# Kernel tuning notes

Hardware: AMD Instinct MI355X
Metric: run time of the kernel (lower is better)

## Reference

```python
import math
import jax, jax.numpy as jnp
import numpy as np

B, L, D = 2, 2048, 512
H, DK, RANK, NH = 8, 64, 32, 1
K_MAX = 64
BANDWIDTH = 8.0
N_BUCKETS = 16


def setup_inputs() -> dict:
    key = jax.random.key(0)
    ks = jax.random.split(key, 14)
    s = 0.02
    return {
        "query": jax.random.normal(ks[0], (B, L, D), jnp.float32),
        "key": jax.random.normal(ks[1], (B, L, D), jnp.float32),
        "value": jax.random.normal(ks[2], (B, L, D), jnp.float32),
        "Wq": jax.random.normal(ks[3], (D, H * DK), jnp.float32) * s,
        "bq": jnp.zeros((H * DK,), jnp.float32),
        "Wk": jax.random.normal(ks[4], (D, H * DK), jnp.float32) * s,
        "bk": jnp.zeros((H * DK,), jnp.float32),
        "Wv": jax.random.normal(ks[5], (D, H * DK), jnp.float32) * s,
        "bv": jnp.zeros((H * DK,), jnp.float32),
        "U": jax.random.normal(ks[6], (H, DK, RANK), jnp.float32) * s,
        "V": jax.random.normal(ks[7], (H, RANK, D), jnp.float32) * s,
        "rv": jax.random.normal(ks[8], (H, DK, NH), jnp.float32),  # LSH random vectors (buffer)
        "Wo": jax.random.normal(ks[9], (H * D, D), jnp.float32) * s,
        "bo": jnp.zeros((D,), jnp.float32),
    }


def _lsh_hash(x, r):
    # binary quantize then bucketed floor hash: [B,L,dk] @ [dk,nh] -> [B,L,nh]
    xb = (x > 0).astype(x.dtype)
    return jnp.floor((xb @ r) / BANDWIDTH) % N_BUCKETS


def reference(query, key, value, Wq, bq, Wk, bk, Wv, bv, U, V, rv, Wo, bo):
    Bq, Lq, Dm = query.shape
    nheads, dk = U.shape[0], U.shape[1]
    q = (query @ Wq + bq).reshape(Bq, Lq, nheads, dk).transpose(0, 2, 1, 3)  # [B,H,L,dk]
    k = (key @ Wk + bk).reshape(Bq, Lq, nheads, dk).transpose(0, 2, 1, 3)
    v = (value @ Wv + bv).reshape(Bq, Lq, nheads, dk).transpose(0, 2, 1, 3)
    scale = math.sqrt(dk)  # optimized_sqrt(d_key), d_key power of two

    head_outputs = []
    for h in range(nheads):
        qh, kh, vh = q[:, h], k[:, h], v[:, h]  # [B,L,dk]
        qhash = _lsh_hash(qh, rv[h])  # [B,L,nh]
        khash = _lsh_hash(kh, rv[h])
        # [B,L,L] candidate match matrix (all hashes equal)
        matches = (qhash[:, :, None, :] == khash[:, None, :, :]).all(-1)
        # first K_MAX matching key indices in ascending order (== torch nonzero order)
        order = jnp.argsort(jnp.logical_not(matches), axis=-1, stable=True)
        cand = order[:, :, :K_MAX]  # [B,L,k_max]
        valid = jnp.take_along_axis(matches, cand, axis=-1)  # [B,L,k_max]
        ckeys = jnp.take_along_axis(kh[:, None, :, :], cand[..., None], axis=2)  # [B,L,k_max,dk]
        cvals = jnp.take_along_axis(vh[:, None, :, :], cand[..., None], axis=2)
        sim = jnp.einsum('bld,blkd->blk', qh, ckeys) / scale
        sim = jnp.where(valid, sim, -jnp.inf)
        attn = jax.nn.softmax(sim, axis=-1)  # invalid slots get exactly 0 weight
        # attention-weighted sum then low-rank up-projection (linear, so commutes
        # with the weighted sum; avoids the [B,L,k_max,d_model] intermediate)
        ctx = jnp.einsum('blk,blkd->bld', attn, cvals)  # [B,L,dk]
        head_outputs.append((ctx @ U[h]) @ V[h])  # [B,L,d_model]

    concat = jnp.concatenate(head_outputs, axis=-1)  # [B,L,H*d_model]
    return concat @ Wo + bo
```

## Files before the change

### kernel.cpp

```cpp
#include <hip/hip_runtime.h>
#include <math.h>

#define Bb 2
#define Ll 2048
#define Dd 512
#define Hh 8
#define DKq 64
#define NBUCK 16
#define KMAX 64
#define MAX_ITEMS 1280

__device__ __forceinline__ void gl_lds16(const float* g, float* l) {
  __builtin_amdgcn_global_load_lds(
      (const __attribute__((address_space(1))) void*)g,
      (__attribute__((address_space(3))) void*)l, 16, 0, 0);
}

__global__ __launch_bounds__(128) void proj_kernel(
    const float* __restrict__ Xq, const float* __restrict__ Xk, const float* __restrict__ Xv,
    const float* __restrict__ Wq, const float* __restrict__ Wk, const float* __restrict__ Wv,
    const float* __restrict__ bq, const float* __restrict__ bk, const float* __restrict__ bv,
    float* __restrict__ qb, float* __restrict__ kb, float* __restrict__ vb)
{
  const float *X, *W, *bias; float* dst;
  if (blockIdx.z == 0)      { X=Xq; W=Wq; bias=bq; dst=qb; }
  else if (blockIdx.z == 1) { X=Xk; W=Wk; bias=bk; dst=kb; }
  else                      { X=Xv; W=Wv; bias=bv; dst=vb; }
  __shared__ float As[2][64 * 32];
  __shared__ float Bs[2][32 * 128];
  const int tid = threadIdx.x;
  const int m0 = blockIdx.y * 64;
  const int n0 = blockIdx.x * 128;
  const int tx = tid & 15, ty = tid >> 4;
  const int lane = tid & 63, wid = tid >> 6;

  const float* aSrc[4];
  #pragma unroll
  for (int j = 0; j < 4; j++) {
    int jj = wid * 4 + j;
    aSrc[j] = X + (size_t)(m0 + 8*jj + (lane >> 3)) * 512 + (((lane & 7) ^ jj) << 2);
  }
  const float* bSrc[8];
  #pragma unroll
  for (int j = 0; j < 8; j++) {
    int jj = wid * 8 + j;
    bSrc[j] = W + (size_t)(2*jj + (lane >> 5)) * 512 + n0 + ((lane & 31) << 2);
  }

  #pragma unroll
  for (int j = 0; j < 4; j++) gl_lds16(aSrc[j],            &As[0][(wid*4+j)*256]);
  #pragma unroll
  for (int j = 0; j < 8; j++) gl_lds16(bSrc[j],            &Bs[0][(wid*8+j)*256]);
  __syncthreads();

  float acc[8][8] = {};
  for (int t = 0; t < 16; t++) {
    const int cur = t & 1;
    if (t < 15) {
      const int k0 = (t + 1) * 32;
      #pragma unroll
      for (int j = 0; j < 4; j++) gl_lds16(aSrc[j] + k0,              &As[cur^1][(wid*4+j)*256]);
      #pragma unroll
      for (int j = 0; j < 8; j++) gl_lds16(bSrc[j] + (size_t)k0*512,  &Bs[cur^1][(wid*8+j)*256]);
    }
    const float* Ac = &As[cur][0];
    const float* Bc = &Bs[cur][0];
    #pragma unroll
    for (int kk4 = 0; kk4 < 8; kk4++) {
      float4 a[8];
      #pragma unroll
      for (int i = 0; i < 8; i++)
        a[i] = *(const float4*)&Ac[(ty*8 + i)*32 + ((kk4 ^ ty) << 2)];
      #pragma unroll
      for (int s = 0; s < 4; s++) {
        const int kk = kk4*4 + s;
        float4 b0 = *(const float4*)&Bc[kk*128 + tx*4];
        float4 b1 = *(const float4*)&Bc[kk*128 + 64 + tx*4];
        #pragma unroll
        for (int i = 0; i < 8; i++) {
          const float as = (s==0) ? a[i].x : (s==1) ? a[i].y : (s==2) ? a[i].z : a[i].w;
          acc[i][0] += as * b0.x;  acc[i][1] += as * b0.y;
          acc[i][2] += as * b0.z;  acc[i][3] += as * b0.w;
          acc[i][4] += as * b1.x;  acc[i][5] += as * b1.y;
          acc[i][6] += as * b1.z;  acc[i][7] += as * b1.w;
        }
      }
    }
    __syncthreads();
  }

  const int head0 = n0 >> 6;
  const int d0 = tx * 4;
  #pragma unroll
  for (int i = 0; i < 8; i++) {
    int m = m0 + ty*8 + i;
    int b = m >> 11, l = m & 2047;
    float* drow0 = &dst[(((size_t)b*Hh + head0)*Ll + l)*DKq];
    float* drow1 = &dst[(((size_t)b*Hh + head0 + 1)*Ll + l)*DKq];
    #pragma unroll
    for (int j = 0; j < 4; j++) drow0[d0 + j] = acc[i][j]   + bias[n0 + tx*4 + j];
    #pragma unroll
    for (int j = 0; j < 4; j++) drow1[d0 + j] = acc[i][4+j] + bias[n0 + 64 + tx*4 + j];
  }
}

__global__ __launch_bounds__(256) void hash_kernel(
    const float* __restrict__ qb, const float* __restrict__ kb,
    const float* __restrict__ rv, int* __restrict__ qhash, int* __restrict__ khash)
{
  int gwave = (blockIdx.x * blockDim.x + threadIdx.x) >> 6;
  int lane = threadIdx.x & 63;
  const int NR = Bb * Hh * Ll;
  if (gwave >= 2 * NR) return;
  int isK = gwave >= NR;
  int row = isK ? gwave - NR : gwave;
  int h = (row >> 11) & 7;
  const float* src = isK ? kb : qb;
  float x = src[(size_t)row * DKq + lane];
  float r = rv[h * DKq + lane];
  float v = (x > 0.0f) ? r : 0.0f;
  #pragma unroll
  for (int off = 32; off; off >>= 1) v += __shfl_xor(v, off);
  if (lane == 0) {
    float fb = floorf(v * 0.125f);
    int ib = (int)fb;
    int bucket = ib & 15;
    (isK ? khash : qhash)[row] = bucket;
  }
}

__global__ __launch_bounds__(64) void kcand_kernel(
    const int* __restrict__ khash, int* __restrict__ kcand, int* __restrict__ kcount)
{
  int bh = blockIdx.x >> 4;
  int bucket = blockIdx.x & 15;
  int lane = threadIdx.x;
  const int* kh = &khash[bh * Ll];
  int* cl = &kcand[(size_t)blockIdx.x * KMAX];
  int total = 0;
  for (int c0 = 0; c0 < Ll && total < KMAX; c0 += 64) {
    int hv = kh[c0 + lane];
    unsigned long long m = __ballot(hv == bucket);
    int pre = __popcll(m & ((1ULL << lane) - 1ULL));
    if (hv == bucket && total + pre < KMAX) cl[total + pre] = c0 + lane;
    total += __popcll(m);
  }
  if (lane == 0) kcount[blockIdx.x] = total < KMAX ? total : KMAX;
}

__global__ __launch_bounds__(256) void qlist_kernel(
    const int* __restrict__ qhash, int* __restrict__ qoff, int* __restrict__ qlist)
{
  int bh = blockIdx.x;
  __shared__ int cnt[NBUCK], cur[NBUCK], off[NBUCK + 1];
  if (threadIdx.x < NBUCK) cnt[threadIdx.x] = 0;
  __syncthreads();
  const int* qh = &qhash[bh * Ll];
  for (int l = threadIdx.x; l < Ll; l += 256) atomicAdd(&cnt[qh[l]], 1);
  __syncthreads();
  if (threadIdx.x == 0) {
    int s = 0;
    for (int i = 0; i < NBUCK; i++) { off[i] = s; cur[i] = s; s += cnt[i]; }
    off[NBUCK] = s;
  }
  __syncthreads();
  if (threadIdx.x < NBUCK + 1) qoff[bh * (NBUCK + 1) + threadIdx.x] = off[threadIdx.x];
  for (int l = threadIdx.x; l < Ll; l += 256) {
    int p = atomicAdd(&cur[qh[l]], 1);
    qlist[bh * Ll + p] = l;
  }
}

__global__ __launch_bounds__(256) void worklist_kernel(
    const int* __restrict__ qoff, const int* __restrict__ kcount,
    int4* __restrict__ items, int* __restrict__ nitems)
{
  int t = threadIdx.x;
  int bh = t >> 4, bucket = t & 15;
  int o0 = qoff[bh * 17 + bucket], o1 = qoff[bh * 17 + bucket + 1];
  int cnt = kcount[t];
  int nq = o1 - o0;
  int n = (cnt > 0) ? ((nq + 31) >> 5) : 0;
  __shared__ int sc[256];
  sc[t] = n;
  __syncthreads();
  for (int off = 1; off < 256; off <<= 1) {
    int v = (t >= off) ? sc[t - off] : 0;
    __syncthreads();
    sc[t] += v;
    __syncthreads();
  }
  int start = sc[t] - n;
  for (int i = 0; i < n; i++) {
    int q0 = 32 * i;
    int qn = nq - q0; if (qn > 32) qn = 32;
    items[start + i] = make_int4(t, o0 + q0, qn, cnt);
  }
  if (t == 255) nitems[0] = sc[255];
}

__device__ __forceinline__ void lds_fence() {
  asm volatile("s_waitcnt lgkmcnt(0)" ::: "memory");
  __builtin_amdgcn_sched_barrier(0);
}

__global__ __launch_bounds__(256, 2) void attn_kernel(
    const float* __restrict__ qb, const float* __restrict__ kb, const float* __restrict__ vb,
    const int* __restrict__ qlist, const int* __restrict__ kcand,
    const int4* __restrict__ items, const int* __restrict__ nitems,
    float* __restrict__ ctx)
{
  __shared__ float qs_all[4][32 * 64];
  __shared__ float sa_all[4][64];
  const int wid = threadIdx.x >> 6, lane = threadIdx.x & 63;
  const int idx = blockIdx.x * 4 + wid;
  if (idx >= nitems[0]) return;
  const int4 it = items[idx];
  const int code = it.x, qstart = it.y, qn = it.z, cnt = it.w;
  const int bh = code >> 4;
  float* qs = qs_all[wid];
  float* sa = sa_all[wid];

  const float* qbh = qb + (size_t)bh * Ll * DKq;
  const float* kbh = kb + (size_t)bh * Ll * DKq;
  const float* vbh = vb + (size_t)bh * Ll * DKq;

  int qidx_v = (lane < qn)  ? qlist[bh * Ll + qstart + lane] : 0;
  int cidx_v = (lane < cnt) ? kcand[(size_t)code * KMAX + lane] : 0;

  float4 kr[16];
  {
    const float4* krow = (const float4*)kbh + (size_t)cidx_v * 16;
    #pragma unroll
    for (int i = 0; i < 16; i++) kr[i] = krow[i];
  }
  float vt[64];
  #pragma unroll
  for (int c = 0; c < 64; c++) {
    int rowc = __shfl(cidx_v, c);
    vt[c] = vbh[(size_t)rowc * DKq + lane];
  }
  #pragma unroll
  for (int i = 0; i < 8; i++) {
    int f = lane + 64 * i;
    int r = f >> 4, c4 = f & 15;
    int qrow = __shfl(qidx_v, r);
    float4 qv = *((const float4*)qbh + (size_t)qrow * 16 + c4);
    *(float4*)&qs[r * 64 + c4 * 4] = qv;
  }
  lds_fence();

  const int b = bh >> 3, h = bh & 7;
  const float4* qs4 = (const float4*)qs;
  const float4* sa4 = (const float4*)sa;

  for (int j = 0; j < qn; j++) {
    float s0 = 0.f, s1 = 0.f, s2 = 0.f, s3 = 0.f;
    #pragma unroll
    for (int i = 0; i < 16; i += 4) {
      float4 q0 = qs4[j * 16 + i + 0];
      float4 q1 = qs4[j * 16 + i + 1];
      float4 q2 = qs4[j * 16 + i + 2];
      float4 q3 = qs4[j * 16 + i + 3];
      s0 += q0.x*kr[i+0].x + q0.y*kr[i+0].y + q0.z*kr[i+0].z + q0.w*kr[i+0].w;
      s1 += q1.x*kr[i+1].x + q1.y*kr[i+1].y + q1.z*kr[i+1].z + q1.w*kr[i+1].w;
      s2 += q2.x*kr[i+2].x + q2.y*kr[i+2].y + q2.z*kr[i+2].z + q2.w*kr[i+2].w;
      s3 += q3.x*kr[i+3].x + q3.y*kr[i+3].y + q3.z*kr[i+3].z + q3.w*kr[i+3].w;
    }
    float s = ((s0 + s1) + (s2 + s3)) * 0.125f;
    s = (lane < cnt) ? s : -INFINITY;
    float m = s;
    #pragma unroll
    for (int off = 32; off; off >>= 1) m = fmaxf(m, __shfl_xor(m, off));
    float e = __expf(s - m);
    float sum = e;
    #pragma unroll
    for (int off = 32; off; off >>= 1) sum += __shfl_xor(sum, off);
    lds_fence();
    sa[lane] = e;
    lds_fence();
    float c0 = 0.f, c1 = 0.f, c2 = 0.f, c3 = 0.f;
    #pragma unroll
    for (int i = 0; i < 16; i++) {
      float4 a = sa4[i];
      c0 += a.x * vt[4*i + 0];
      c1 += a.y * vt[4*i + 1];
      c2 += a.z * vt[4*i + 2];
      c3 += a.w * vt[4*i + 3];
    }
    float ctxd = ((c0 + c1) + (c2 + c3)) / sum;
    int qrow = __shfl(qidx_v, j);
    ctx[((size_t)(b * Ll + qrow)) * 512 + h * 64 + lane] = ctxd;
  }
}

__global__ __launch_bounds__(256) void uv_kernel(
    const float* __restrict__ U, const float* __restrict__ V, float* __restrict__ T)
{
  int idx = blockIdx.x * 256 + threadIdx.x;
  int n = idx & 511, dk = (idx >> 9) & 63, h = idx >> 15;
  float acc = 0.f;
  #pragma unroll
  for (int r = 0; r < 32; r++)
    acc += U[((size_t)h * 64 + dk) * 32 + r] * V[((size_t)h * 32 + r) * 512 + n];
  T[idx] = acc;
}

__global__ __launch_bounds__(256) void m_kernel(
    const float* __restrict__ T, const float* __restrict__ Wo, float* __restrict__ Mf)
{
  __shared__ float Ts[16][68];
  __shared__ float Ws[16][68];
  const int h = blockIdx.y;
  const int n0 = blockIdx.x * 64;
  const int tid = threadIdx.x;
  const int tx = tid & 15, ty = tid >> 4;
  float acc[4][4] = {};
  for (int k0 = 0; k0 < 512; k0 += 16) {
    {
      int r = tid >> 2, cg = (tid & 3) << 2;
      float4 a = *(const float4*)&T[((size_t)(h*64 + r))*512 + k0 + cg];
      Ts[cg+0][r]=a.x; Ts[cg+1][r]=a.y; Ts[cg+2][r]=a.z; Ts[cg+3][r]=a.w;
    }
    {
      int row = tid >> 4, c4 = tid & 15;
      *(float4*)&Ws[row][c4*4] = *(const float4*)&Wo[((size_t)(h*512 + k0 + row))*512 + n0 + c4*4];
    }
    __syncthreads();
    #pragma unroll
    for (int kk = 0; kk < 16; kk++) {
      float4 a0 = *(const float4*)&Ts[kk][ty*4];
      float4 b0 = *(const float4*)&Ws[kk][tx*4];
      float av[4] = {a0.x,a0.y,a0.z,a0.w};
      float bw[4] = {b0.x,b0.y,b0.z,b0.w};
      #pragma unroll
      for (int i=0;i<4;i++)
        #pragma unroll
        for (int j=0;j<4;j++) acc[i][j] += av[i]*bw[j];
    }
    __syncthreads();
  }
  #pragma unroll
  for (int i=0;i<4;i++) {
    int row = h*64 + ty*4 + i;
    #pragma unroll
    for (int j=0;j<4;j++)
      Mf[(size_t)row * 512 + n0 + tx*4 + j] = acc[i][j];
  }
}

__global__ __launch_bounds__(128) void out_gemm(
    const float* __restrict__ A, const float* __restrict__ Bm,
    const float* __restrict__ bias, float* __restrict__ C)
{
  __shared__ float As[32][68];
  __shared__ float Bs[32][68];
  const int tid = threadIdx.x;
  const int m0 = blockIdx.y * 64, n0 = blockIdx.x * 64;
  const int tx = tid & 15, ty = tid >> 4;

  float4 ar[4], br[4];
  #pragma unroll
  for (int i = 0; i < 4; i++) {
    int g = i * 128 + tid, row = g >> 3, c4 = g & 7;
    ar[i] = *(const float4*)&A[(size_t)(m0 + row) * 512 + c4 * 4];
  }
  #pragma unroll
  for (int i = 0; i < 4; i++) {
    int g = i * 128 + tid, row = g >> 4, c4 = g & 15;
    br[i] = *(const float4*)&Bm[(size_t)row * 512 + n0 + c4 * 4];
  }

  float acc[8][4] = {};
  for (int k0 = 0; k0 < 512; k0 += 32) {
    __syncthreads();
    #pragma unroll
    for (int i = 0; i < 4; i++) {
      int g = i * 128 + tid, row = g >> 3, c4 = g & 7;
      int mswz = ((c4 >> 1) & 1) << 3;
      As[c4*4+0][(row ^ mswz)] = ar[i].x;
      As[c4*4+1][(row ^ mswz)] = ar[i].y;
      As[c4*4+2][(row ^ mswz)] = ar[i].z;
      As[c4*4+3][(row ^ mswz)] = ar[i].w;
    }
    #pragma unroll
    for (int i = 0; i < 4; i++) {
      int g = i * 128 + tid, row = g >> 4, c4 = g & 15;
      *(float4*)&Bs[row][c4*4] = br[i];
    }
    __syncthreads();
    if (k0 + 32 < 512) {
      #pragma unroll
      for (int i = 0; i < 4; i++) {
        int g = i * 128 + tid, row = g >> 3, c4 = g & 7;
        ar[i] = *(const float4*)&A[(size_t)(m0 + row) * 512 + (k0 + 32) + c4 * 4];
      }
      #pragma unroll
      for (int i = 0; i < 4; i++) {
        int g = i * 128 + tid, row = g >> 4, c4 = g & 15;
        br[i] = *(const float4*)&Bm[(size_t)(k0 + 32 + row) * 512 + n0 + c4 * 4];
      }
    }
    #pragma unroll
    for (int kk = 0; kk < 32; kk++) {
      const int mswz = ((kk >> 3) & 1) << 3;
      const int mb = (ty * 8) ^ mswz;
      float4 a0 = *(const float4*)&As[kk][mb];
      float4 a1 = *(const float4*)&As[kk][mb + 4];
      float4 b0 = *(const float4*)&Bs[kk][tx*4];
      float av[8] = {a0.x,a0.y,a0.z,a0.w,a1.x,a1.y,a1.z,a1.w};
      float bw[4] = {b0.x,b0.y,b0.z,b0.w};
      #pragma unroll
      for (int i=0;i<8;i++)
        #pragma unroll
        for (int j=0;j<4;j++) acc[i][j] += av[i]*bw[j];
    }
  }
  #pragma unroll
  for (int i=0;i<8;i++) {
    int m = m0 + ty*8 + i;
    #pragma unroll
    for (int j=0;j<4;j++) {
      int n = n0 + tx*4 + j;
      C[(size_t)m * 512 + n] = acc[i][j] + bias[n];
    }
  }
}

extern "C" void kernel_launch(void* const* d_in, const int* in_sizes, int n_in,
                              void* d_out, int out_size, void* d_ws, size_t ws_size,
                              hipStream_t stream)
{
  const float* query = (const float*)d_in[0];
  const float* key   = (const float*)d_in[1];
  const float* value = (const float*)d_in[2];
  const float* Wq = (const float*)d_in[3];
  const float* bq = (const float*)d_in[4];
  const float* Wk = (const float*)d_in[5];
  const float* bk = (const float*)d_in[6];
  const float* Wv = (const float*)d_in[7];
  const float* bv = (const float*)d_in[8];
  const float* U  = (const float*)d_in[9];
  const float* V  = (const float*)d_in[10];
  const float* rv = (const float*)d_in[11];
  const float* Wo = (const float*)d_in[12];
  const float* bo = (const float*)d_in[13];
  float* out = (float*)d_out;

  float* ws = (float*)d_ws;
  const size_t NQKV = (size_t)Bb * Hh * Ll * DKq;
  float* qb   = ws;
  float* kb   = qb + NQKV;
  float* vb   = kb + NQKV;
  float* ctx  = vb + NQKV;
  float* T    = ctx + NQKV;
  float* Mf   = T + (size_t)Hh * DKq * 512;
  int* qhash  = (int*)(Mf + 512 * 512);
  int* khash  = qhash + Bb * Hh * Ll;
  int* kcand  = khash + Bb * Hh * Ll;
  int* kcount = kcand + Bb * Hh * NBUCK * KMAX;
  int* qoff   = kcount + Bb * Hh * NBUCK;
  int* qlist  = qoff + Bb * Hh * (NBUCK + 1);
  int4* items = (int4*)(qlist + Bb * Hh * Ll);
  int* nitems = (int*)(items + MAX_ITEMS);

  proj_kernel<<<dim3(4, 64, 3), 128, 0, stream>>>(query, key, value,
                                                  Wq, Wk, Wv, bq, bk, bv,
                                                  qb, kb, vb);
  hash_kernel<<<(2 * Bb * Hh * Ll * 64) / 256, 256, 0, stream>>>(qb, kb, rv, qhash, khash);
  kcand_kernel<<<Bb * Hh * NBUCK, 64, 0, stream>>>(khash, kcand, kcount);
  qlist_kernel<<<Bb * Hh, 256, 0, stream>>>(qhash, qoff, qlist);
  worklist_kernel<<<1, 256, 0, stream>>>(qoff, kcount, items, nitems);
  attn_kernel<<<MAX_ITEMS / 4, 256, 0, stream>>>(qb, kb, vb, qlist, kcand,
                                                 items, nitems, ctx);
  uv_kernel<<<(Hh * DKq * 512) / 256, 256, 0, stream>>>(U, V, T);
  m_kernel<<<dim3(8, 8), 256, 0, stream>>>(T, Wo, Mf);
  out_gemm<<<dim3(8, 64), 128, 0, stream>>>(ctx, Mf, bo, out);
}
```

Baseline: 288.7 us.

## Use single-wave blocks with smaller tiles and vmcnt waits in QKV projection GEMM

Restructures the QKV projection GEMM so each block is a single 64-thread wave computing a 32x128 tile with a K-step of 16. The launch grid doubles along M. Because each block is one wave, the block-wide __syncthreads barriers are replaced by explicit s_waitcnt vmcnt waits on the asynchronous global-to-LDS loads. The aim is more blocks in flight and no cross-wave barrier stalls. The cost is less reuse per loaded tile and twice as many K iterations.

```diff
diff --git a/kernel.cpp b/kernel.cpp
--- a/kernel.cpp
+++ b/kernel.cpp
@@ -16,7 +16,13 @@
       (__attribute__((address_space(3))) void*)l, 16, 0, 0);
 }
 
-__global__ __launch_bounds__(128) void proj_kernel(
+#define VM_WAIT(N)                                                \
+  do {                                                            \
+    asm volatile("s_waitcnt vmcnt(" #N ")" ::: "memory");         \
+    __builtin_amdgcn_sched_barrier(0);                            \
+  } while (0)
+
+__global__ __launch_bounds__(64) void proj_kernel(
     const float* __restrict__ Xq, const float* __restrict__ Xk, const float* __restrict__ Xv,
     const float* __restrict__ Wq, const float* __restrict__ Wk, const float* __restrict__ Wv,
     const float* __restrict__ bq, const float* __restrict__ bk, const float* __restrict__ bv,
@@ -26,51 +32,56 @@
   if (blockIdx.z == 0)      { X=Xq; W=Wq; bias=bq; dst=qb; }
   else if (blockIdx.z == 1) { X=Xk; W=Wk; bias=bk; dst=kb; }
   else                      { X=Xv; W=Wv; bias=bv; dst=vb; }
-  __shared__ float As[2][64 * 32];
-  __shared__ float Bs[2][32 * 128];
-  const int tid = threadIdx.x;
-  const int m0 = blockIdx.y * 64;
+  __shared__ float As[2][32 * 16];
+  __shared__ float Bs[2][16 * 128];
+  const int lane = threadIdx.x;
+  const int m0 = blockIdx.y * 32;
   const int n0 = blockIdx.x * 128;
-  const int tx = tid & 15, ty = tid >> 4;
-  const int lane = tid & 63, wid = tid >> 6;
-
-  const float* aSrc[4];
-  #pragma unroll
-  for (int j = 0; j < 4; j++) {
-    int jj = wid * 4 + j;
-    aSrc[j] = X + (size_t)(m0 + 8*jj + (lane >> 3)) * 512 + (((lane & 7) ^ jj) << 2);
+  const int tx = lane & 15, ty = lane >> 4;
+
+  const float* aSrc[2];
+  #pragma unroll
+  for (int j = 0; j < 2; j++) {
+    int row  = 16*j + (lane >> 2);
+    int key  = (row >> 3) & 3;
+    int sK4  = (lane & 3) ^ key;
+    aSrc[j] = X + (size_t)(m0 + row) * 512 + (sK4 << 2);
   }
   const float* bSrc[8];
   #pragma unroll
   for (int j = 0; j < 8; j++) {
-    int jj = wid * 8 + j;
-    bSrc[j] = W + (size_t)(2*jj + (lane >> 5)) * 512 + n0 + ((lane & 31) << 2);
-  }
-
-  #pragma unroll
-  for (int j = 0; j < 4; j++) gl_lds16(aSrc[j],            &As[0][(wid*4+j)*256]);
-  #pragma unroll
-  for (int j = 0; j < 8; j++) gl_lds16(bSrc[j],            &Bs[0][(wid*8+j)*256]);
-  __syncthreads();
+    int krow = 2*j + (lane >> 5);
+    bSrc[j] = W + (size_t)krow * 512 + n0 + ((lane & 31) << 2);
+  }
+
+  #pragma unroll
+  for (int j = 0; j < 2; j++) gl_lds16(aSrc[j], &As[0][j*256]);
+  #pragma unroll
+  for (int j = 0; j < 8; j++) gl_lds16(bSrc[j], &Bs[0][j*256]);
 
   float acc[8][8] = {};
-  for (int t = 0; t < 16; t++) {
+  for (int t = 0; t < 32; t++) {
     const int cur = t & 1;
-    if (t < 15) {
-      const int k0 = (t + 1) * 32;
-      #pragma unroll
-      for (int j = 0; j < 4; j++) gl_lds16(aSrc[j] + k0,              &As[cur^1][(wid*4+j)*256]);
-      #pragma unroll
-      for (int j = 0; j < 8; j++) gl_lds16(bSrc[j] + (size_t)k0*512,  &Bs[cur^1][(wid*8+j)*256]);
-    }
+    if (t < 31) {
+      const int ks = (t + 1) * 16;
+      const int nb = cur ^ 1;
+      #pragma unroll
+      for (int j = 0; j < 2; j++) gl_lds16(aSrc[j] + ks,              &As[nb][j*256]);
+      #pragma unroll
+      for (int j = 0; j < 8; j++) gl_lds16(bSrc[j] + (size_t)ks*512,  &Bs[nb][j*256]);
+      VM_WAIT(10);
+    } else {
+      VM_WAIT(0);
+    }
+
     const float* Ac = &As[cur][0];
     const float* Bc = &Bs[cur][0];
     #pragma unroll
-    for (int kk4 = 0; kk4 < 8; kk4++) {
+    for (int kk4 = 0; kk4 < 4; kk4++) {
       float4 a[8];
       #pragma unroll
       for (int i = 0; i < 8; i++)
-        a[i] = *(const float4*)&Ac[(ty*8 + i)*32 + ((kk4 ^ ty) << 2)];
+        a[i] = *(const float4*)&Ac[(ty*8 + i)*16 + ((kk4 ^ ty) << 2)];
       #pragma unroll
       for (int s = 0; s < 4; s++) {
         const int kk = kk4*4 + s;
@@ -78,7 +89,8 @@
         float4 b1 = *(const float4*)&Bc[kk*128 + 64 + tx*4];
         #pragma unroll
         for (int i = 0; i < 8; i++) {
-          const float as = (s==0) ? a[i].x : (s==1) ? a[i].y : (s==2) ? a[i].z : a[i].w;
+          const float as = (s==0) ? a[i].x : (s==1) ? a[i].y
+                         : (s==2) ? a[i].z : a[i].w;
           acc[i][0] += as * b0.x;  acc[i][1] += as * b0.y;
           acc[i][2] += as * b0.z;  acc[i][3] += as * b0.w;
           acc[i][4] += as * b1.x;  acc[i][5] += as * b1.y;
@@ -86,7 +98,6 @@
         }
       }
     }
-    __syncthreads();
   }
 
   const int head0 = n0 >> 6;
@@ -464,7 +475,7 @@
   int4* items = (int4*)(qlist + Bb * Hh * Ll);
   int* nitems = (int*)(items + MAX_ITEMS);
 
-  proj_kernel<<<dim3(4, 64, 3), 128, 0, stream>>>(query, key, value,
+  proj_kernel<<<dim3(4, 128, 3), 64, 0, stream>>>(query, key, value,
                                                   Wq, Wk, Wv, bq, bk, bv,
                                                   qb, kb, vb);
   hash_kernel<<<(2 * Bb * Hh * Ll * 64) / 256, 256, 0, stream>>>(qb, kb, rv, qhash, khash);
```

Result: faster. 263.7 us (-8.7%).
